# Optimization experiments

Hardware: AMD Instinct MI355X
Metric: run time of the kernel (lower is better)

## Reference

```python
import jax, jax.numpy as jnp
import numpy as np

SEQ_LEN, BATCH, VOCAB, EMB, HID, NLAYERS = 64, 128, 10000, 1024, 1024, 2


def setup_inputs() -> dict:
    key = jax.random.key(0)
    ks = jax.random.split(key, 12)
    u = lambda k, shape: jax.random.uniform(k, shape, jnp.float32, -0.1, 0.1)
    inputs = jax.random.randint(ks[0], (SEQ_LEN, BATCH), 0, VOCAB)
    hidden = jnp.zeros((NLAYERS, BATCH, HID), jnp.float32)
    emb_table = u(ks[1], (VOCAB, EMB))
    # gate weights: in_features = EMB(+)HID == 2*HID since EMB==HID; stacked over layers
    Wr = u(ks[2], (NLAYERS, 2 * HID, HID)); br = jnp.zeros((NLAYERS, HID), jnp.float32)
    Wz = u(ks[3], (NLAYERS, 2 * HID, HID)); bz = jnp.zeros((NLAYERS, HID), jnp.float32)
    Wg = u(ks[4], (NLAYERS, 2 * HID, HID)); bg = jnp.zeros((NLAYERS, HID), jnp.float32)
    Wout = u(ks[5], (HID, VOCAB)); bout = jnp.zeros((VOCAB,), jnp.float32)
    return {"inputs": inputs, "hidden": hidden, "emb_table": emb_table,
            "Wr": Wr, "br": br, "Wz": Wz, "bz": bz, "Wg": Wg, "bg": bg,
            "Wout": Wout, "bout": bout}


def reference(inputs, hidden, emb_table, Wr, br, Wz, bz, Wg, bg, Wout, bout):
    # inputs: [T, B] int ids; hidden: [L, B, H]
    x = emb_table[inputs]  # [T, B, E]
    L = Wr.shape[0]

    def step(h, x_t):
        inp = x_t
        new_h = []
        for l in range(L):
            cat = jnp.concatenate([inp, h[l]], axis=-1)            # [B, 2H]
            r = jnp.tanh(cat @ Wr[l] + br[l])                      # tanh gate (as in source)
            z = jnp.tanh(cat @ Wz[l] + bz[l])
            cat2 = jnp.concatenate([inp, r * h[l]], axis=-1)
            h_tild = jnp.tanh(cat2 @ Wg[l] + bg[l])
            hn = (1.0 - z) * h[l] + z * h_tild
            inp = hn
            new_h.append(hn)
        logits_t = jnp.tanh(inp @ Wout + bout)                     # Tanh on logits (as in source)
        return jnp.stack(new_h), logits_t

    h_final, logits = jax.lax.scan(step, hidden, x)
    return logits, h_final
```

## Files before the change

### kernel.cpp

```cpp
#include <hip/hip_runtime.h>

#define T_STEPS 64
#define BATCH   128
#define HID     1024
#define VOCAB   10000
#define VPAD    10240
#define NSPLIT  8
#define KCHUNK  256
#define TKK     64

typedef unsigned short ushort_t;
typedef __attribute__((ext_vector_type(8))) short bf16x8_t;
typedef __attribute__((ext_vector_type(4))) float f32x4_t;

__device__ inline unsigned short f2bf(float f) {
    unsigned int u = __float_as_uint(f);
    u += 0x7fffu + ((u >> 16) & 1u);
    return (unsigned short)(u >> 16);
}

__global__ void init_h(const float* __restrict__ hidden,
                       float* __restrict__ h0, float* __restrict__ h1)
{
    int i = blockIdx.x * blockDim.x + threadIdx.x;
    if (i < BATCH * HID) {
        h0[i] = hidden[i];
        h1[i] = hidden[BATCH * HID + i];
    }
}

__global__ void final_h(const float* __restrict__ h0, const float* __restrict__ h1,
                        float* __restrict__ out)
{
    int i = blockIdx.x * blockDim.x + threadIdx.x;
    if (i < BATCH * HID) {
        out[i] = h0[i];
        out[BATCH * HID + i] = h1[i];
    }
}

__global__ __launch_bounds__(256)
void gather_kernel(const int* __restrict__ ids, const float* __restrict__ emb,
                   float* __restrict__ xemb)
{
    const int row = blockIdx.x;
    const int c4 = threadIdx.x * 4;
    float4 v = *(const float4*)&emb[(size_t)ids[row] * HID + c4];
    *(float4*)&xemb[(size_t)row * HID + c4] = v;
}

__global__ __launch_bounds__(256)
void woutT_kernel(const float* __restrict__ Wout, ushort_t* __restrict__ WT)
{
    __shared__ float ld[32][33];
    const int v0 = blockIdx.x * 32, k0 = blockIdx.y * 32;
    const int r = threadIdx.x >> 3;
    const int c4 = (threadIdx.x & 7) * 4;
    #pragma unroll
    for (int q = 0; q < 4; ++q) {
        int v = v0 + c4 + q;
        float val = 0.0f;
        if (v < VOCAB) val = Wout[(size_t)(k0 + r) * VOCAB + v];
        ld[c4 + q][r] = val;
    }
    __syncthreads();
    ushort4 o;
    o.x = f2bf(ld[r][c4 + 0]);
    o.y = f2bf(ld[r][c4 + 1]);
    o.z = f2bf(ld[r][c4 + 2]);
    o.w = f2bf(ld[r][c4 + 3]);
    *(ushort4*)&WT[(size_t)(v0 + r) * HID + k0 + c4] = o;
}

__global__ __launch_bounds__(256)
void agemm_kernel(const float* __restrict__ xemb_t0,
                  const float* __restrict__ h0, const float* __restrict__ h1,
                  const float* __restrict__ Wr, const float* __restrict__ Wz,
                  float* __restrict__ part_rz, int do0, int do1)
{
    const int layer = blockIdx.z;
    if (layer == 0 && !do0) return;
    if (layer == 1 && !do1) return;

    __shared__ float As[TKK][132];
    __shared__ float Bs[TKK][36];
    const int tid = threadIdx.x;
    const int tx4 = (tid & 7) * 4;
    const int ty4 = (tid >> 3) * 4;
    const int j0 = blockIdx.x * 32;
    const int kbase = blockIdx.y * KCHUNK;

    const float* W = ((j0 < HID) ? Wr : Wz) + (size_t)layer * (2 * HID * HID);
    const int jc = j0 & (HID - 1);
    const float* A_lo = layer ? h0 : xemb_t0;
    const float* A_hi = layer ? h1 : h0;

    float acc[4][4] = {};

    for (int kt = 0; kt < KCHUNK; kt += TKK) {
        #pragma unroll
        for (int i = 0; i < 8; ++i) {
            int e = (i & 3) * 256 + tid;
            int r = e >> 3;
            int kc = (e & 7) * 4 + (i >> 2) * 32;
            int kg = kbase + kt + kc;
            const float* src = (kg < HID) ? A_lo : A_hi;
            float4 v = *(const float4*)&src[(size_t)r * HID + (kg & (HID - 1))];
            As[kc + 0][r] = v.x; As[kc + 1][r] = v.y;
            As[kc + 2][r] = v.z; As[kc + 3][r] = v.w;
        }
        #pragma unroll
        for (int i = 0; i < 2; ++i) {
            int e = i * 256 + tid;
            int kr = e >> 3;
            int c = (e & 7) * 4;
            *(float4*)&Bs[kr][c] =
                *(const float4*)&W[(size_t)(kbase + kt + kr) * HID + jc + c];
        }
        __syncthreads();
        #pragma unroll
        for (int kk = 0; kk < TKK; ++kk) {
            float a[4], b[4];
            *(float4*)a = *(const float4*)&As[kk][ty4];
            *(float4*)b = *(const float4*)&Bs[kk][tx4];
            #pragma unroll
            for (int i = 0; i < 4; ++i)
                #pragma unroll
                for (int j = 0; j < 4; ++j)
                    acc[i][j] += a[i] * b[j];
        }
        __syncthreads();
    }

    float* dst = part_rz + (size_t)(layer * NSPLIT + blockIdx.y) * (BATCH * 2 * HID);
    #pragma unroll
    for (int i = 0; i < 4; ++i) {
        int b = ty4 + i;
        float4 v; v.x = acc[i][0]; v.y = acc[i][1]; v.z = acc[i][2]; v.w = acc[i][3];
        *(float4*)&dst[(size_t)b * 2048 + j0 + tx4] = v;
    }
}

__global__ __launch_bounds__(256)
void aact_kernel(const float* __restrict__ part_rz,
                 const float* __restrict__ br,
                 float* __restrict__ rmat0, float* __restrict__ rmat1,
                 int do0, int do1)
{
    const int layer = blockIdx.y;
    if (layer == 0 && !do0) return;
    if (layer == 1 && !do1) return;
    const int idx4 = (blockIdx.x * 256 + threadIdx.x) * 4;
    const int b = idx4 >> 10, j = idx4 & (HID - 1);
    const float* p = part_rz + (size_t)layer * NSPLIT * (BATCH * 2 * HID)
                   + (size_t)b * 2048 + j;
    float4 s = {0.f, 0.f, 0.f, 0.f};
    #pragma unroll
    for (int sp = 0; sp < NSPLIT; ++sp) {
        float4 v = *(const float4*)&p[(size_t)sp * (BATCH * 2 * HID)];
        s.x += v.x; s.y += v.y; s.z += v.z; s.w += v.w;
    }
    float4 bb = *(const float4*)&br[layer * HID + j];
    float4 r;
    r.x = tanhf(s.x + bb.x); r.y = tanhf(s.y + bb.y);
    r.z = tanhf(s.z + bb.z); r.w = tanhf(s.w + bb.w);
    *(float4*)&(layer ? rmat1 : rmat0)[idx4] = r;
}

__global__ __launch_bounds__(256)
void bgemm_kernel(const float* __restrict__ xemb_t0,
                  const float* __restrict__ h0, const float* __restrict__ h1,
                  const float* __restrict__ rmat0, const float* __restrict__ rmat1,
                  const float* __restrict__ Wg,
                  float* __restrict__ part_g, int do0, int do1)
{
    const int layer = blockIdx.z;
    if (layer == 0 && !do0) return;
    if (layer == 1 && !do1) return;

    __shared__ float As[TKK][132];
    __shared__ float Bs[TKK][36];
    const int tid = threadIdx.x;
    const int tx4 = (tid & 7) * 4;
    const int ty4 = (tid >> 3) * 4;
    const int j0 = blockIdx.x * 32;
    const int kbase = blockIdx.y * KCHUNK;

    const float* W = Wg + (size_t)layer * (2 * HID * HID);
    const float* A_lo = layer ? h0 : xemb_t0;
    const float* A_hi = layer ? h1 : h0;
    const float* R    = layer ? rmat1 : rmat0;

    float acc[4][4] = {};

    for (int kt = 0; kt < KCHUNK; kt += TKK) {
        #pragma unroll
        for (int i = 0; i < 8; ++i) {
            int e = (i & 3) * 256 + tid;
            int r = e >> 3;
            int kc = (e & 7) * 4 + (i >> 2) * 32;
            int kg = kbase + kt + kc;
            int km = kg & (HID - 1);
            float4 v;
            if (kg < HID) {
                v = *(const float4*)&A_lo[(size_t)r * HID + km];
            } else {
                float4 rv = *(const float4*)&R[(size_t)r * HID + km];
                float4 hv = *(const float4*)&A_hi[(size_t)r * HID + km];
                v.x = rv.x * hv.x; v.y = rv.y * hv.y;
                v.z = rv.z * hv.z; v.w = rv.w * hv.w;
            }
            As[kc + 0][r] = v.x; As[kc + 1][r] = v.y;
            As[kc + 2][r] = v.z; As[kc + 3][r] = v.w;
        }
        #pragma unroll
        for (int i = 0; i < 2; ++i) {
            int e = i * 256 + tid;
            int kr = e >> 3;
            int c = (e & 7) * 4;
            *(float4*)&Bs[kr][c] =
                *(const float4*)&W[(size_t)(kbase + kt + kr) * HID + j0 + c];
        }
        __syncthreads();
        #pragma unroll
        for (int kk = 0; kk < TKK; ++kk) {
            float a[4], b[4];
            *(float4*)a = *(const float4*)&As[kk][ty4];
            *(float4*)b = *(const float4*)&Bs[kk][tx4];
            #pragma unroll
            for (int i = 0; i < 4; ++i)
                #pragma unroll
                for (int j = 0; j < 4; ++j)
                    acc[i][j] += a[i] * b[j];
        }
        __syncthreads();
    }

    float* dst = part_g + (size_t)(layer * NSPLIT + blockIdx.y) * (BATCH * HID);
    #pragma unroll
    for (int i = 0; i < 4; ++i) {
        int b = ty4 + i;
        float4 v; v.x = acc[i][0]; v.y = acc[i][1]; v.z = acc[i][2]; v.w = acc[i][3];
        *(float4*)&dst[(size_t)b * HID + j0 + tx4] = v;
    }
}

__global__ __launch_bounds__(256)
void bact_kernel(const float* __restrict__ part_rz, const float* __restrict__ part_g,
                 const float* __restrict__ bz, const float* __restrict__ bg,
                 float* __restrict__ h0, float* __restrict__ h1,
                 ushort_t* __restrict__ h1bf, int t1, int do0, int do1)
{
    const int layer = blockIdx.y;
    if (layer == 0 && !do0) return;
    if (layer == 1 && !do1) return;
    const int idx4 = (blockIdx.x * 256 + threadIdx.x) * 4;
    const int b = idx4 >> 10, j = idx4 & (HID - 1);

    const float* pz = part_rz + (size_t)layer * NSPLIT * (BATCH * 2 * HID)
                    + (size_t)b * 2048 + HID + j;
    float4 sz = {0.f, 0.f, 0.f, 0.f};
    #pragma unroll
    for (int sp = 0; sp < NSPLIT; ++sp) {
        float4 v = *(const float4*)&pz[(size_t)sp * (BATCH * 2 * HID)];
        sz.x += v.x; sz.y += v.y; sz.z += v.z; sz.w += v.w;
    }
    float4 bzv = *(const float4*)&bz[layer * HID + j];
    float4 z;
    z.x = tanhf(sz.x + bzv.x); z.y = tanhf(sz.y + bzv.y);
    z.z = tanhf(sz.z + bzv.z); z.w = tanhf(sz.w + bzv.w);

    const float* pg = part_g + (size_t)layer * NSPLIT * (BATCH * HID) + idx4;
    float4 sg = {0.f, 0.f, 0.f, 0.f};
    #pragma unroll
    for (int sp = 0; sp < NSPLIT; ++sp) {
        float4 v = *(const float4*)&pg[(size_t)sp * (BATCH * HID)];
        sg.x += v.x; sg.y += v.y; sg.z += v.z; sg.w += v.w;
    }
    float4 bgv = *(const float4*)&bg[layer * HID + j];
    float4 g;
    g.x = tanhf(sg.x + bgv.x); g.y = tanhf(sg.y + bgv.y);
    g.z = tanhf(sg.z + bgv.z); g.w = tanhf(sg.w + bgv.w);

    float* h = layer ? h1 : h0;
    float4 hv = *(const float4*)&h[idx4];
    float4 hn;
    hn.x = (1.0f - z.x) * hv.x + z.x * g.x;
    hn.y = (1.0f - z.y) * hv.y + z.y * g.y;
    hn.z = (1.0f - z.z) * hv.z + z.z * g.z;
    hn.w = (1.0f - z.w) * hv.w + z.w * g.w;
    *(float4*)&h[idx4] = hn;

    if (layer == 1) {
        ushort4 o;
        o.x = f2bf(hn.x); o.y = f2bf(hn.y); o.z = f2bf(hn.z); o.w = f2bf(hn.w);
        *(ushort4*)&h1bf[(size_t)t1 * (BATCH * HID) + idx4] = o;
    }
}

typedef const unsigned int __attribute__((address_space(1)))* gptr1_t;
typedef unsigned int __attribute__((address_space(3)))* lptr3_t;

__global__ __launch_bounds__(256)
void logits_mfma_kernel(const ushort_t* __restrict__ Abf,
                        const ushort_t* __restrict__ BT,
                        const float* __restrict__ bout,
                        float* __restrict__ out)
{
    __shared__ ushort_t As[128 * 64];
    __shared__ ushort_t Bs[128 * 64];
    const int tid = threadIdx.x;
    const int wave = tid >> 6, lane = tid & 63;
    const int m0 = blockIdx.y * 128, n0 = blockIdx.x * 128;
    const int wr = wave >> 1, wc = wave & 1;

    const int srow = lane >> 3;
    const int sch = (lane & 7) ^ (srow & 7);
    const int lrow = lane & 15, lhi = lane >> 4;

    f32x4_t acc[4][4] = {};

    for (int k0 = 0; k0 < HID; k0 += 64) {
        #pragma unroll
        for (int i = 0; i < 4; ++i) {
            int issue = wave * 4 + i;
            int row = issue * 8 + srow;
            const ushort_t* ga = Abf + (size_t)(m0 + row) * HID + k0 + sch * 8;
            const ushort_t* gb = BT + (size_t)(n0 + row) * HID + k0 + sch * 8;
#if defined(__has_builtin) && __has_builtin(__builtin_amdgcn_global_load_lds)
            __builtin_amdgcn_global_load_lds((gptr1_t)(const void*)ga,
                                             (lptr3_t)(void*)(As + issue * 512), 16, 0, 0);
            __builtin_amdgcn_global_load_lds((gptr1_t)(const void*)gb,
                                             (lptr3_t)(void*)(Bs + issue * 512), 16, 0, 0);
#else
            *(bf16x8_t*)(As + issue * 512 + lane * 8) = *(const bf16x8_t*)ga;
            *(bf16x8_t*)(Bs + issue * 512 + lane * 8) = *(const bf16x8_t*)gb;
#endif
        }
        __syncthreads();

        bf16x8_t af[4][2], bfm[4][2];
        const char* Ab = (const char*)As;
        const char* Bb = (const char*)Bs;
        #pragma unroll
        for (int m = 0; m < 4; ++m) {
            int row = wr * 64 + m * 16 + lrow;
            #pragma unroll
            for (int ks = 0; ks < 2; ++ks) {
                int off = row * 128 + (((ks * 4 + lhi) ^ (lrow & 7)) * 16);
                af[m][ks] = *(const bf16x8_t*)(Ab + off);
            }
        }
        #pragma unroll
        for (int n = 0; n < 4; ++n) {
            int row = wc * 64 + n * 16 + lrow;
            #pragma unroll
            for (int ks = 0; ks < 2; ++ks) {
                int off = row * 128 + (((ks * 4 + lhi) ^ (lrow & 7)) * 16);
                bfm[n][ks] = *(const bf16x8_t*)(Bb + off);
            }
        }
        #pragma unroll
        for (int m = 0; m < 4; ++m)
            #pragma unroll
            for (int n = 0; n < 4; ++n)
                #pragma unroll
                for (int ks = 0; ks < 2; ++ks)
                    acc[m][n] = __builtin_amdgcn_mfma_f32_16x16x32_bf16(
                        af[m][ks], bfm[n][ks], acc[m][n], 0, 0, 0);
        __syncthreads();
    }

    #pragma unroll
    for (int m = 0; m < 4; ++m) {
        int row = m0 + wr * 64 + m * 16 + lhi * 4;
        #pragma unroll
        for (int n = 0; n < 4; ++n) {
            int col = n0 + wc * 64 + n * 16 + lrow;
            if (col < VOCAB) {
                float bo = bout[col];
                #pragma unroll
                for (int q = 0; q < 4; ++q)
                    out[(size_t)(row + q) * VOCAB + col] = tanhf(acc[m][n][q] + bo);
            }
        }
    }
}

extern "C" void kernel_launch(void* const* d_in, const int* in_sizes, int n_in,
                              void* d_out, int out_size, void* d_ws, size_t ws_size,
                              hipStream_t stream)
{
    const int*   inputs = (const int*)  d_in[0];
    const float* hidden = (const float*)d_in[1];
    const float* emb    = (const float*)d_in[2];
    const float* Wr     = (const float*)d_in[3];
    const float* br     = (const float*)d_in[4];
    const float* Wz     = (const float*)d_in[5];
    const float* bz     = (const float*)d_in[6];
    const float* Wg     = (const float*)d_in[7];
    const float* bg     = (const float*)d_in[8];
    const float* Wout   = (const float*)d_in[9];
    const float* bout   = (const float*)d_in[10];
    float* out = (float*)d_out;

    const size_t BH = BATCH * HID;

    float* ws = (float*)d_ws;
    float* h0      = ws;
    float* h1      = h0 + BH;
    float* rmat0   = h1 + BH;
    float* rmat1   = rmat0 + BH;
    float* part_rz = rmat1 + BH;
    float* part_g  = part_rz + 2 * NSPLIT * (BATCH * 2 * HID);
    float* xemb    = part_g + 2 * NSPLIT * (BATCH * HID);
    ushort_t* h1bf = (ushort_t*)(xemb + (size_t)T_STEPS * BH);
    ushort_t* WT   = h1bf + (size_t)T_STEPS * BH;

    init_h<<<(int)(BH + 255) / 256, 256, 0, stream>>>(hidden, h0, h1);
    gather_kernel<<<T_STEPS * BATCH, 256, 0, stream>>>(inputs, emb, xemb);
    woutT_kernel<<<dim3(VPAD / 32, HID / 32), 256, 0, stream>>>(Wout, WT);

    for (int s = 0; s <= T_STEPS; ++s) {
        int do0 = (s < T_STEPS) ? 1 : 0;
        int do1 = (s >= 1) ? 1 : 0;
        const float* xemb_t0 = xemb + (size_t)s * BH;
        agemm_kernel<<<dim3(64, NSPLIT, 2), 256, 0, stream>>>(
            xemb_t0, h0, h1, Wr, Wz, part_rz, do0, do1);
        aact_kernel<<<dim3(128, 2), 256, 0, stream>>>(
            part_rz, br, rmat0, rmat1, do0, do1);
        bgemm_kernel<<<dim3(32, NSPLIT, 2), 256, 0, stream>>>(
            xemb_t0, h0, h1, rmat0, rmat1, Wg, part_g, do0, do1);
        bact_kernel<<<dim3(128, 2), 256, 0, stream>>>(
            part_rz, part_g, bz, bg, h0, h1, h1bf, s - 1, do0, do1);
    }

    final_h<<<(int)(BH + 255) / 256, 256, 0, stream>>>(
        h0, h1, out + (size_t)T_STEPS * BATCH * VOCAB);

    logits_mfma_kernel<<<dim3(VPAD / 128, 8192 / 128), 256, 0, stream>>>(
        h1bf, WT, bout, out);
}
```

Measured before the change: 5.012 ms.

## Read GRU gate weights as wave-uniform scalar loads instead of LDS tiles

The recurrent gate GEMM kernels now use 512 threads. Each wave owns 64 batch rows and 8 output columns, so its weight addresses are the same across lanes and the compiler can emit scalar loads. The weight tile no longer goes through shared memory. Only the activation tile is staged, row-major, and results are transposed through LDS for coalesced stores. The aim is to cut LDS traffic and syncs on the weight operand, at the cost of fewer accumulators per thread and reliance on scalar-cache bandwidth.

Result: slower. 6.874 ms (+37.2%).

```diff
diff --git a/kernel.cpp b/kernel.cpp
--- a/kernel.cpp
+++ b/kernel.cpp
@@ -7,7 +7,6 @@
 #define VPAD    10240
 #define NSPLIT  8
 #define KCHUNK  256
-#define TKK     64
 
 typedef unsigned short ushort_t;
 typedef __attribute__((ext_vector_type(8))) short bf16x8_t;
@@ -72,21 +71,22 @@
     *(ushort4*)&WT[(size_t)(v0 + r) * HID + k0 + c4] = o;
 }
 
-__global__ __launch_bounds__(256)
-void agemm_kernel(const float* __restrict__ xemb_t0,
-                  const float* __restrict__ h0, const float* __restrict__ h1,
-                  const float* __restrict__ Wr, const float* __restrict__ Wz,
-                  float* __restrict__ part_rz, int do0, int do1)
+__global__ __launch_bounds__(512)
+void agemm_s(const float* __restrict__ xemb_t0,
+             const float* __restrict__ h0, const float* __restrict__ h1,
+             const float* __restrict__ Wr, const float* __restrict__ Wz,
+             float* __restrict__ part_rz, int do0, int do1)
 {
     const int layer = blockIdx.z;
     if (layer == 0 && !do0) return;
     if (layer == 1 && !do1) return;
 
-    __shared__ float As[TKK][132];
-    __shared__ float Bs[TKK][36];
+    __shared__ float As[128][68];
     const int tid = threadIdx.x;
-    const int tx4 = (tid & 7) * 4;
-    const int ty4 = (tid >> 3) * 4;
+    const int wuni = __builtin_amdgcn_readfirstlane(tid >> 6);
+    const int lane = tid & 63;
+    const int row  = (wuni & 1) * 64 + lane;
+    const int colb = (wuni >> 1) * 8;
     const int j0 = blockIdx.x * 32;
     const int kbase = blockIdx.y * KCHUNK;
 
@@ -95,49 +95,52 @@
     const float* A_lo = layer ? h0 : xemb_t0;
     const float* A_hi = layer ? h1 : h0;
 
-    float acc[4][4] = {};
-
-    for (int kt = 0; kt < KCHUNK; kt += TKK) {
-        #pragma unroll
-        for (int i = 0; i < 8; ++i) {
-            int e = (i & 3) * 256 + tid;
-            int r = e >> 3;
-            int kc = (e & 7) * 4 + (i >> 2) * 32;
-            int kg = kbase + kt + kc;
+    float acc[8] = {};
+
+    for (int kt0 = 0; kt0 < KCHUNK; kt0 += 64) {
+        const int ktg = kbase + kt0;
+        #pragma unroll
+        for (int i = 0; i < 4; ++i) {
+            int f = i * 512 + tid;
+            int r = f >> 4;
+            int c4 = (f & 15) * 4;
+            int kg = ktg + c4;
             const float* src = (kg < HID) ? A_lo : A_hi;
-            float4 v = *(const float4*)&src[(size_t)r * HID + (kg & (HID - 1))];
-            As[kc + 0][r] = v.x; As[kc + 1][r] = v.y;
-            As[kc + 2][r] = v.z; As[kc + 3][r] = v.w;
-        }
-        #pragma unroll
-        for (int i = 0; i < 2; ++i) {
-            int e = i * 256 + tid;
-            int kr = e >> 3;
-            int c = (e & 7) * 4;
-            *(float4*)&Bs[kr][c] =
-                *(const float4*)&W[(size_t)(kbase + kt + kr) * HID + jc + c];
-        }
-        __syncthreads();
-        #pragma unroll
-        for (int kk = 0; kk < TKK; ++kk) {
-            float a[4], b[4];
-            *(float4*)a = *(const float4*)&As[kk][ty4];
-            *(float4*)b = *(const float4*)&Bs[kk][tx4];
+            *(float4*)&As[r][c4] =
+                *(const float4*)&src[(size_t)r * HID + (kg & (HID - 1))];
+        }
+        __syncthreads();
+        #pragma unroll
+        for (int c = 0; c < 16; ++c) {
+            f32x4_t a4 = *(const f32x4_t*)&As[row][c * 4];
             #pragma unroll
-            for (int i = 0; i < 4; ++i)
+            for (int q = 0; q < 4; ++q) {
+                const float* __restrict__ wk =
+                    W + (size_t)(ktg + c * 4 + q) * HID + jc + colb;
                 #pragma unroll
-                for (int j = 0; j < 4; ++j)
-                    acc[i][j] += a[i] * b[j];
-        }
-        __syncthreads();
-    }
+                for (int cc = 0; cc < 8; ++cc)
+                    acc[cc] += a4[q] * wk[cc];
+            }
+        }
+        __syncthreads();
+    }
+
+    float (*As33)[33] = (float(*)[33])As;
+    #pragma unroll
+    for (int cc = 0; cc < 8; ++cc)
+        As33[row][colb + cc] = acc[cc];
+    __syncthreads();
 
     float* dst = part_rz + (size_t)(layer * NSPLIT + blockIdx.y) * (BATCH * 2 * HID);
     #pragma unroll
-    for (int i = 0; i < 4; ++i) {
-        int b = ty4 + i;
-        float4 v; v.x = acc[i][0]; v.y = acc[i][1]; v.z = acc[i][2]; v.w = acc[i][3];
-        *(float4*)&dst[(size_t)b * 2048 + j0 + tx4] = v;
+    for (int i = 0; i < 2; ++i) {
+        int e = i * 512 + tid;
+        int r = e >> 3;
+        int c4 = (e & 7) * 4;
+        float4 v;
+        v.x = As33[r][c4 + 0]; v.y = As33[r][c4 + 1];
+        v.z = As33[r][c4 + 2]; v.w = As33[r][c4 + 3];
+        *(float4*)&dst[(size_t)r * 2048 + j0 + c4] = v;
     }
 }
 
@@ -167,22 +170,23 @@
     *(float4*)&(layer ? rmat1 : rmat0)[idx4] = r;
 }
 
-__global__ __launch_bounds__(256)
-void bgemm_kernel(const float* __restrict__ xemb_t0,
-                  const float* __restrict__ h0, const float* __restrict__ h1,
-                  const float* __restrict__ rmat0, const float* __restrict__ rmat1,
-                  const float* __restrict__ Wg,
-                  float* __restrict__ part_g, int do0, int do1)
+__global__ __launch_bounds__(512)
+void bgemm_s(const float* __restrict__ xemb_t0,
+             const float* __restrict__ h0, const float* __restrict__ h1,
+             const float* __restrict__ rmat0, const float* __restrict__ rmat1,
+             const float* __restrict__ Wg,
+             float* __restrict__ part_g, int do0, int do1)
 {
     const int layer = blockIdx.z;
     if (layer == 0 && !do0) return;
     if (layer == 1 && !do1) return;
 
-    __shared__ float As[TKK][132];
-    __shared__ float Bs[TKK][36];
+    __shared__ float As[128][68];
     const int tid = threadIdx.x;
-    const int tx4 = (tid & 7) * 4;
-    const int ty4 = (tid >> 3) * 4;
+    const int wuni = __builtin_amdgcn_readfirstlane(tid >> 6);
+    const int lane = tid & 63;
+    const int row  = (wuni & 1) * 64 + lane;
+    const int colb = (wuni >> 1) * 8;
     const int j0 = blockIdx.x * 32;
     const int kbase = blockIdx.y * KCHUNK;
 
@@ -191,15 +195,16 @@
     const float* A_hi = layer ? h1 : h0;
     const float* R    = layer ? rmat1 : rmat0;
 
-    float acc[4][4] = {};
-
-    for (int kt = 0; kt < KCHUNK; kt += TKK) {
-        #pragma unroll
-        for (int i = 0; i < 8; ++i) {
-            int e = (i & 3) * 256 + tid;
-            int r = e >> 3;
-            int kc = (e & 7) * 4 + (i >> 2) * 32;
-            int kg = kbase + kt + kc;
+    float acc[8] = {};
+
+    for (int kt0 = 0; kt0 < KCHUNK; kt0 += 64) {
+        const int ktg = kbase + kt0;
+        #pragma unroll
+        for (int i = 0; i < 4; ++i) {
+            int f = i * 512 + tid;
+            int r = f >> 4;
+            int c4 = (f & 15) * 4;
+            int kg = ktg + c4;
             int km = kg & (HID - 1);
             float4 v;
             if (kg < HID) {
@@ -210,38 +215,40 @@
                 v.x = rv.x * hv.x; v.y = rv.y * hv.y;
                 v.z = rv.z * hv.z; v.w = rv.w * hv.w;
             }
-            As[kc + 0][r] = v.x; As[kc + 1][r] = v.y;
-            As[kc + 2][r] = v.z; As[kc + 3][r] = v.w;
-        }
-        #pragma unroll
-        for (int i = 0; i < 2; ++i) {
-            int e = i * 256 + tid;
-            int kr = e >> 3;
-            int c = (e & 7) * 4;
-            *(float4*)&Bs[kr][c] =
-                *(const float4*)&W[(size_t)(kbase + kt + kr) * HID + j0 + c];
-        }
-        __syncthreads();
-        #pragma unroll
-        for (int kk = 0; kk < TKK; ++kk) {
-            float a[4], b[4];
-            *(float4*)a = *(const float4*)&As[kk][ty4];
-            *(float4*)b = *(const float4*)&Bs[kk][tx4];
+            *(float4*)&As[r][c4] = v;
+        }
+        __syncthreads();
+        #pragma unroll
+        for (int c = 0; c < 16; ++c) {
+            f32x4_t a4 = *(const f32x4_t*)&As[row][c * 4];
             #pragma unroll
-            for (int i = 0; i < 4; ++i)
+            for (int q = 0; q < 4; ++q) {
+                const float* __restrict__ wk =
+                    W + (size_t)(ktg + c * 4 + q) * HID + j0 + colb;
                 #pragma unroll
-                for (int j = 0; j < 4; ++j)
-                    acc[i][j] += a[i] * b[j];
-        }
-        __syncthreads();
-    }
+                for (int cc = 0; cc < 8; ++cc)
+                    acc[cc] += a4[q] * wk[cc];
+            }
+        }
+        __syncthreads();
+    }
+
+    float (*As33)[33] = (float(*)[33])As;
+    #pragma unroll
+    for (int cc = 0; cc < 8; ++cc)
+        As33[row][colb + cc] = acc[cc];
+    __syncthreads();
 
     float* dst = part_g + (size_t)(layer * NSPLIT + blockIdx.y) * (BATCH * HID);
     #pragma unroll
-    for (int i = 0; i < 4; ++i) {
-        int b = ty4 + i;
-        float4 v; v.x = acc[i][0]; v.y = acc[i][1]; v.z = acc[i][2]; v.w = acc[i][3];
-        *(float4*)&dst[(size_t)b * HID + j0 + tx4] = v;
+    for (int i = 0; i < 2; ++i) {
+        int e = i * 512 + tid;
+        int r = e >> 3;
+        int c4 = (e & 7) * 4;
+        float4 v;
+        v.x = As33[r][c4 + 0]; v.y = As33[r][c4 + 1];
+        v.z = As33[r][c4 + 2]; v.w = As33[r][c4 + 3];
+        *(float4*)&dst[(size_t)r * HID + j0 + c4] = v;
     }
 }
 
@@ -425,11 +432,11 @@
         int do0 = (s < T_STEPS) ? 1 : 0;
         int do1 = (s >= 1) ? 1 : 0;
         const float* xemb_t0 = xemb + (size_t)s * BH;
-        agemm_kernel<<<dim3(64, NSPLIT, 2), 256, 0, stream>>>(
+        agemm_s<<<dim3(64, NSPLIT, 2), 512, 0, stream>>>(
             xemb_t0, h0, h1, Wr, Wz, part_rz, do0, do1);
         aact_kernel<<<dim3(128, 2), 256, 0, stream>>>(
             part_rz, br, rmat0, rmat1, do0, do1);
-        bgemm_kernel<<<dim3(32, NSPLIT, 2), 256, 0, stream>>>(
+        bgemm_s<<<dim3(32, NSPLIT, 2), 512, 0, stream>>>(
             xemb_t0, h0, h1, rmat0, rmat1, Wg, part_g, do0, do1);
         bact_kernel<<<dim3(128, 2), 256, 0, stream>>>(
             part_rz, part_g, bz, bg, h0, h1, h1bf, s - 1, do0, do1);
```
